# Optimization experiments

Hardware: AMD Instinct MI355X
Metric: run time of the kernel (lower is better)

The kernel has to match this reference:

```python
import jax, jax.numpy as jnp
import numpy as np

B, S, SR, H, NH, L, V, FF = 4, 512, 512, 1024, 16, 6, 32000, 4096
HD = H // NH  # 64
PAD = 2


def setup_inputs() -> dict:
    key = jax.random.key(0)
    ks = jax.random.split(key, 40)
    f32 = jnp.float32

    def n(k, shape, scale=0.02):
        return jax.random.normal(k, shape, f32) * scale

    encoder_outputs = jax.random.normal(ks[0], (B, SR, H), f32)
    decoder_input = jax.random.randint(ks[1], (B, S), 0, V)
    decoder_input = jnp.where(decoder_input == PAD, 3, decoder_input)
    decoder_input = decoder_input.at[:, S - 64:].set(PAD).at[:, 0].set(5)
    encoder_input = jax.random.randint(ks[2], (B, SR), 0, V)
    encoder_input = jnp.where(encoder_input == PAD, 3, encoder_input)
    encoder_input = encoder_input.at[:, SR - 64:].set(PAD)

    emb = jax.random.normal(ks[3], (V, H), f32).at[PAD].set(0.0)  # padding_idx=2 row is zero

    return {
        'encoder_outputs': encoder_outputs,
        'decoder_input': decoder_input,
        'encoder_input': encoder_input,
        'emb': emb,
        'wq1': n(ks[4], (L, H, H)), 'bq1': jnp.zeros((L, H), f32),
        'wk1': n(ks[5], (L, H, H)), 'bk1': jnp.zeros((L, H), f32),
        'wv1': n(ks[6], (L, H, H)), 'bv1': jnp.zeros((L, H), f32),
        'wo1': n(ks[7], (L, H, H)), 'bo1': jnp.zeros((L, H), f32),
        'pos1': jax.random.normal(ks[8], (L, 2 * S - 1, HD), f32),  # torch.randn init
        'wq2': n(ks[9], (L, H, H)), 'bq2': jnp.zeros((L, H), f32),
        'wk2': n(ks[10], (L, H, H)), 'bk2': jnp.zeros((L, H), f32),
        'wv2': n(ks[11], (L, H, H)), 'bv2': jnp.zeros((L, H), f32),
        'wo2': n(ks[12], (L, H, H)), 'bo2': jnp.zeros((L, H), f32),
        'ln1g': jnp.ones((L, H), f32), 'ln1b': jnp.zeros((L, H), f32),
        'ln2g': jnp.ones((L, H), f32), 'ln2b': jnp.zeros((L, H), f32),
        'ln3g': jnp.ones((L, H), f32), 'ln3b': jnp.zeros((L, H), f32),
        'wf1': n(ks[13], (L, H, FF)), 'bf1': jnp.zeros((L, FF), f32),
        'wf2': n(ks[14], (L, FF, H)), 'bf2': jnp.zeros((L, H), f32),
        'wout': n(ks[15], (H, V)), 'bout': jnp.zeros((V,), f32),
    }


def _split_heads(x):
    b, l, _ = x.shape
    return x.reshape(b, l, NH, HD).transpose(0, 2, 1, 3)  # b h l d


def _layer_norm(x, g, b):
    m = x.mean(-1, keepdims=True)
    v = ((x - m) ** 2).mean(-1, keepdims=True)
    return (x - m) / jnp.sqrt(v + 1e-5) * g + b


def _skew(q, P):
    # Transformer-XL style relative-position skew. q: [b,h,S,d] (already scaled), P: [2S-1,d]
    b = q.shape[0]
    pe = jnp.einsum('bhid,jd->bhij', q, P)                 # [b,h,S,2S-1]
    pe = jnp.pad(pe, ((0, 0), (0, 0), (0, 0), (0, 1)))      # [b,h,S,2S]
    pe = pe.reshape(b, NH, 2 * S * S)
    pe = jnp.pad(pe, ((0, 0), (0, 0), (0, S - 1)))
    pe = pe.reshape(b, NH, S + 1, 2 * S - 1)
    return pe[:, :, :-1, -S:]                               # [b,h,S,S]


def _attention(xq, xkv, wq, bq, wk, bk, wv, bv, wo, bo, pos, add_mask, causal):
    b = xq.shape[0]
    q = _split_heads(xq @ wq + bq) / np.float32(np.sqrt(HD))
    k = _split_heads(xkv @ wk + bk)
    v = _split_heads(xkv @ wv + bv)
    att = jnp.einsum('bhid,bhjd->bhij', q, k)
    if pos is not None:
        att = att + _skew(q, pos)
    if causal:
        i = jnp.arange(S)[:, None]
        j = jnp.arange(att.shape[-1])[None, :]
        att = jnp.where(j > i, -jnp.inf, att)
    if add_mask is not None:
        att = att + add_mask
    s = jax.nn.softmax(att, axis=-1)
    o = jnp.einsum('bhqk,bhkd->bhqd', s, v)
    o = o.transpose(0, 2, 1, 3).reshape(b, S, H)
    return o @ wo + bo


def _forward(encoder_outputs, decoder_input, encoder_input, emb,
             wq1, bq1, wk1, bk1, wv1, bv1, wo1, bo1, pos1,
             wq2, bq2, wk2, bk2, wv2, bv2, wo2, bo2,
             ln1g, ln1b, ln2g, ln2b, ln3g, ln3b,
             wf1, bf1, wf2, bf2, wout, bout):
    self_mask = jnp.where(decoder_input == PAD, -jnp.inf, 0.0)[:, None, None, :]   # [b,1,1,S]
    cross_mask = jnp.where(encoder_input == PAD, -jnp.inf, 0.0)[:, None, None, :]  # [b,1,1,SR]
    x = emb[decoder_input]  # dropout_p=0 -> identity
    for i in range(L):
        a1 = _attention(x, x, wq1[i], bq1[i], wk1[i], bk1[i], wv1[i], bv1[i],
                        wo1[i], bo1[i], pos1[i], self_mask, True)
        x1 = _layer_norm(a1 + x, ln1g[i], ln1b[i])
        a2 = _attention(x1, encoder_outputs, wq2[i], bq2[i], wk2[i], bk2[i], wv2[i], bv2[i],
                        wo2[i], bo2[i], None, cross_mask, False)
        x2 = _layer_norm(a2 + x1, ln2g[i], ln2b[i])
        ff = jax.nn.relu(x2 @ wf1[i] + bf1[i]) @ wf2[i] + bf2[i]
        x = _layer_norm(ff + x2, ln3g[i], ln3b[i])
    return jax.nn.log_softmax(x @ wout + bout, axis=-1)  # [b,S,V]


def reference(encoder_outputs, decoder_input, encoder_input, emb,
              wq1, bq1, wk1, bk1, wv1, bv1, wo1, bo1, pos1,
              wq2, bq2, wk2, bk2, wv2, bv2, wo2, bo2,
              ln1g, ln1b, ln2g, ln2b, ln3g, ln3b,
              wf1, bf1, wf2, bf2, wout, bout):
    return _forward(encoder_outputs, decoder_input, encoder_input, emb,
                    wq1, bq1, wk1, bk1, wv1, bv1, wo1, bo1, pos1,
                    wq2, bq2, wk2, bk2, wv2, bv2, wo2, bo2,
                    ln1g, ln1b, ln2g, ln2b, ln3g, ln3b,
                    wf1, bf1, wf2, bf2, wout, bout)
```

## Files before the change

kernel.cpp:

```cpp
#include <hip/hip_runtime.h>


typedef unsigned short u16;
typedef short s16x8 __attribute__((ext_vector_type(8)));
typedef unsigned short u16x4 __attribute__((ext_vector_type(4)));
typedef unsigned short u16x8 __attribute__((ext_vector_type(8)));
typedef float f32x4 __attribute__((ext_vector_type(4)));

#define PADTOK 2
#define NEG_INF (-__builtin_inff())

static __device__ __forceinline__ u16 f2bf(float f) {
  unsigned u = __float_as_uint(f);
  u += 0x7fffu + ((u >> 16) & 1u);
  return (u16)(u >> 16);
}
static __device__ __forceinline__ float bf2f(u16 h) {
  return __uint_as_float(((unsigned)h) << 16);
}
static __device__ __forceinline__ float f16tof(u16 h) {
  _Float16 x = __builtin_bit_cast(_Float16, h);
  return (float)x;
}
static __device__ __forceinline__ u16 ftof16(float v) {
  _Float16 x = (_Float16)v;
  return __builtin_bit_cast(u16, x);
}
static __device__ __forceinline__ f32x4 mfma16(s16x8 a, s16x8 b, f32x4 c) {
  asm("v_mfma_f32_16x16x32_bf16 %0, %1, %2, %0" : "+v"(c) : "v"(a), "v"(b));
  return c;
}
static __device__ __forceinline__ void gll16(const void* g, void* l) {
  __builtin_amdgcn_global_load_lds((const __attribute__((address_space(1))) void*)g,
                                   (__attribute__((address_space(3))) void*)l, 16, 0, 0);
}
static __device__ __forceinline__ size_t hsidx(int m, int n) {
  return ((size_t)((m >> 9) * 16 + (n >> 6))) * 32768u + (size_t)(m & 511) * 64u + (size_t)(n & 63);
}
static __device__ __forceinline__ size_t vtidx(int m, int n) {
  return ((size_t)((m >> 9) * 16 + (n >> 6))) * 65536u + (size_t)(n & 63) * 512u + (size_t)(m & 511);
}

static __device__ __forceinline__ void raster2(int& bm, int& bn) {
  const int nm = gridDim.y, nn = gridDim.x;
  int bid = blockIdx.y * nn + blockIdx.x;
  const int nwg = nm * nn;
  const int q = nwg >> 3, r = nwg & 7;
  const int x = bid & 7, p = bid >> 3;
  bid = (x < r ? x * (q + 1) : r * (q + 1) + (x - r) * q) + p;
  const int GM = nm < 8 ? nm : 8;
  const int pg = GM * nn;
  const int gi = bid / pg, rem = bid - gi * pg;
  const int left = nm - gi * GM;
  const int gm = left < GM ? left : GM;
  bm = gi * GM + rem % gm;
  bn = rem / gm;
}

template<int EPI, bool BF16OUT, int MFR, bool RELU, bool RESID, bool CSKIP>
__global__ __launch_bounds__(256)
void bgemm(const u16* __restrict__ A, long long sAg,
           const u16* __restrict__ Bt, long long sBg,
           const float* __restrict__ bias, const float* __restrict__ bias2,
           const float* __restrict__ bias3,
           const float* __restrict__ Res,
           void* __restrict__ Cv, u16* __restrict__ C2, u16* __restrict__ C3,
           long long sCg, int ldc, int K, float scale)
{
  constexpr int BM = MFR * 32;
  __shared__ u16 As[BM * 64];
  __shared__ u16 Bs[128 * 64];
  int bmi, bni;
  raster2(bmi, bni);
  const int bm0 = bmi * BM, bn0 = bni * 128;
  if constexpr (CSKIP) {
    if (bn0 > bm0 + BM - 1) return;
  }
  const int g = blockIdx.z;
  const u16* Ag = A + (size_t)g * (size_t)sAg;
  const u16* Bg = Bt + (size_t)g * (size_t)sBg;
  const int tid = threadIdx.x, l = tid & 63, w = tid >> 6;
  const int wm = w >> 1, wn = w & 1;
  const int rsel = l & 15, kg = l >> 4, xs = l & 7;

  f32x4 acc[MFR][4];
#pragma unroll
  for (int i = 0; i < MFR; ++i)
#pragma unroll
    for (int j = 0; j < 4; ++j) acc[i][j] = (f32x4){0.f, 0.f, 0.f, 0.f};

  const int srow = l >> 3;
  const int sch  = (l & 7) ^ srow;
  const u16* Agp = Ag + ((size_t)(bm0 + w * 8 * MFR + srow)) * (size_t)K + sch * 8;
  const u16* Bgp = Bg + ((size_t)(bn0 + w * 32 + srow)) * (size_t)K + sch * 8;
  char* AsL = (char*)As + (w * 8 * MFR) * 128;
  char* BsL = (char*)Bs + (w * 32) * 128;

  for (int k0 = 0; k0 < K; k0 += 64) {
    __syncthreads();
#pragma unroll
    for (int i = 0; i < MFR; ++i)
      gll16(Agp + (size_t)i * 8 * K + k0, AsL + i * 1024);
#pragma unroll
    for (int i = 0; i < 4; ++i)
      gll16(Bgp + (size_t)i * 8 * K + k0, BsL + i * 1024);
    __syncthreads();

    const int arow0 = (wm * (MFR * 16) + rsel) * 128;
    const int brow0 = (wn * 64 + rsel) * 128;
#pragma unroll
    for (int ks = 0; ks < 2; ++ks) {
      const int ch = ((ks * 4 + kg) ^ xs) * 16;
      s16x8 af[MFR], bfr[4];
#pragma unroll
      for (int mf = 0; mf < MFR; ++mf)
        af[mf] = *(const s16x8*)((const char*)As + arow0 + mf * 2048 + ch);
#pragma unroll
      for (int nf = 0; nf < 4; ++nf)
        bfr[nf] = *(const s16x8*)((const char*)Bs + brow0 + nf * 2048 + ch);
#pragma unroll
      for (int mf = 0; mf < MFR; ++mf)
#pragma unroll
        for (int nf = 0; nf < 4; ++nf)
          acc[mf][nf] = mfma16(af[mf], bfr[nf], acc[mf][nf]);
    }
  }

#pragma unroll
  for (int mf = 0; mf < MFR; ++mf) {
#pragma unroll
    for (int nf = 0; nf < 4; ++nf) {
      const int n = bn0 + wn * 64 + nf * 16 + rsel;
      if constexpr (EPI == 3) { if (n >= 64) continue; }
      int sub = 0, nl = n;
      const float* bp = bias;
      if constexpr (EPI == 4) {
        sub = n >> 10; nl = n & 1023;
        bp = (sub == 0) ? bias : (sub == 1) ? bias2 : bias3;
      }
      if constexpr (EPI == 5) {
        sub = n >> 10; nl = n & 1023;
        bp = (sub == 0) ? bias : bias2;
      }
      const float bv = bp ? bp[nl] : 0.f;
      float sc = 1.f;
      if constexpr (EPI == 0 || EPI == 1) sc = scale;
      if constexpr (EPI == 4) sc = (sub == 0) ? scale : 1.f;
#pragma unroll
      for (int e = 0; e < 4; ++e) {
        const int m = bm0 + wm * (MFR * 16) + mf * 16 + kg * 4 + e;
        float v = (acc[mf][nf][e] + bv) * sc;
        if constexpr (RELU) v = fmaxf(v, 0.f);
        if constexpr (RESID) v += Res[(size_t)m * (size_t)ldc + n];
        if constexpr (EPI == 0) {
          const size_t idx = (size_t)g * (size_t)sCg + (size_t)m * (size_t)ldc + n;
          if constexpr (BF16OUT) ((u16*)Cv)[idx] = f2bf(v);
          else                   ((float*)Cv)[idx] = v;
        } else if constexpr (EPI == 1) {
          ((u16*)Cv)[hsidx(m, nl)] = f2bf(v);
        } else if constexpr (EPI == 3) {
          const size_t idx = (size_t)(g >> 4) * 524288u + (size_t)m * 1024u
                           + (size_t)(g & 15) * 64u + n;
          ((u16*)Cv)[idx] = f2bf(v);
        } else if constexpr (EPI == 4) {
          if (sub == 2)      C3[vtidx(m, nl)] = f2bf(v);
          else if (sub == 1) C2[hsidx(m, nl)] = f2bf(v);
          else               ((u16*)Cv)[hsidx(m, nl)] = f2bf(v);
        } else if constexpr (EPI == 5) {
          if (sub == 0) ((u16*)Cv)[hsidx(m, nl)] = f2bf(v);
          else          C2[vtidx(m, nl)] = f2bf(v);
        } else if constexpr (EPI == 6) {
          ((u16*)Cv)[(size_t)m * (size_t)ldc + n] = ftof16(v);
        }
      }
    }
  }
}

static __device__ __forceinline__ void tconv_tile(const float* in, int N,
                                                  u16* out, int K, int k0, int n0) {
  __shared__ u16 L[64][72];
  const int t = threadIdx.x;
  const int rk = t >> 4, cn = (t & 15) * 4;
#pragma unroll
  for (int q = 0; q < 4; ++q) {
    const int kk = k0 + rk + q * 16;
    float4 v = *(const float4*)(in + (size_t)kk * (size_t)N + n0 + cn);
    L[cn + 0][rk + q * 16] = f2bf(v.x);
    L[cn + 1][rk + q * 16] = f2bf(v.y);
    L[cn + 2][rk + q * 16] = f2bf(v.z);
    L[cn + 3][rk + q * 16] = f2bf(v.w);
  }
  __syncthreads();
  const int rn = t >> 2, ck = (t & 3) * 16;
  u16* op = out + (size_t)(n0 + rn) * (size_t)K + k0 + ck;
  *(s16x8*)op       = *(const s16x8*)&L[rn][ck];
  *(s16x8*)(op + 8) = *(const s16x8*)&L[rn][ck + 8];
}

__global__ __launch_bounds__(256)
void conv_layer(const float* w0, const float* w1, const float* w2, const float* w3,
                const float* w4, const float* w5, const float* w6, const float* w7,
                const float* w8, const float* w9, u16* WT) {
  const int b = blockIdx.x;
  const float* in; u16* out; int N, K, kt, nt;
  if (b < 2048) {
    const int j = b >> 8, t = b & 255;
    const float* ws[8] = {w0, w1, w2, w3, w4, w5, w6, w7};
    in = ws[j]; out = WT + (size_t)j * 1048576u; K = 1024; N = 1024;
    kt = t >> 4; nt = t & 15;
  } else if (b < 3072) {
    const int t = b - 2048;
    in = w8; out = WT + 8388608u; K = 1024; N = 4096; kt = t >> 6; nt = t & 63;
  } else {
    const int t = b - 3072;
    in = w9; out = WT + 12582912u; K = 4096; N = 1024; kt = t >> 4; nt = t & 15;
  }
  tconv_tile(in, N, out, K, kt * 64, nt * 64);
}

__global__ __launch_bounds__(256)
void conv_wout(const float* in, u16* out) {
  const int b = blockIdx.x;
  const int kt = b / 500, nt = b % 500;
  tconv_tile(in, 32000, out, 1024, kt * 64, nt * 64);
}

__global__ void conv_bf16(const float* __restrict__ in, u16* __restrict__ out) {
  const int i = (blockIdx.x * 256 + threadIdx.x) * 4;
  float4 v = *(const float4*)(in + i);
  u16x4 h = {f2bf(v.x), f2bf(v.y), f2bf(v.z), f2bf(v.w)};
  *(u16x4*)(out + i) = h;
}

__global__ void conv_pos(const float* __restrict__ pos, u16* __restrict__ posb) {
  const int idx = (blockIdx.x * 256 + threadIdx.x) * 4;
  const int lyr = idx >> 15, rem = idx & 32767;
  float4 v = *(const float4*)(pos + (size_t)lyr * 65472u + rem);
  u16x4 h = {f2bf(v.x), f2bf(v.y), f2bf(v.z), f2bf(v.w)};
  *(u16x4*)(posb + idx) = h;
}

static __device__ __forceinline__ float wred_sum(float v) {
#pragma unroll
  for (int o = 32; o > 0; o >>= 1) v += __shfl_down(v, o, 64);
  return v;
}
static __device__ __forceinline__ float wred_max(float v) {
#pragma unroll
  for (int o = 32; o > 0; o >>= 1) v = fmaxf(v, __shfl_down(v, o, 64));
  return v;
}
static __device__ __forceinline__ float bred_sum(float v, float* sm) {
  const int lane = threadIdx.x & 63, wid = threadIdx.x >> 6;
  v = wred_sum(v);
  if (lane == 0) sm[wid] = v;
  __syncthreads();
  if (threadIdx.x == 0) sm[0] = sm[0] + sm[1] + sm[2] + sm[3];
  __syncthreads();
  const float r = sm[0];
  __syncthreads();
  return r;
}

__global__ void embed_kernel(const int* __restrict__ dec, const float* __restrict__ emb,
                             float* __restrict__ X, u16* __restrict__ Xh) {
  const int m = blockIdx.x, t = threadIdx.x;
  const int tok = dec[m];
  float4 v = ((const float4*)(emb + (size_t)tok * 1024u))[t];
  ((float4*)(X + (size_t)m * 1024u))[t] = v;
  u16x4 h = {f2bf(v.x), f2bf(v.y), f2bf(v.z), f2bf(v.w)};
  *(u16x4*)(Xh + (size_t)m * 1024u + t * 4) = h;
}

__global__ void layernorm_kernel(const float* __restrict__ R,
                                 const float* __restrict__ gw, const float* __restrict__ bw,
                                 float* __restrict__ Y, u16* __restrict__ Yh) {
  __shared__ float sm[4];
  const int m = blockIdx.x, t = threadIdx.x;
  float4 v = ((const float4*)(R + (size_t)m * 1024u))[t];
  float s = v.x + v.y + v.z + v.w;
  s = bred_sum(s, sm);
  const float mean = s * (1.f / 1024.f);
  const float d0 = v.x - mean, d1 = v.y - mean, d2 = v.z - mean, d3 = v.w - mean;
  float q = d0 * d0 + d1 * d1 + d2 * d2 + d3 * d3;
  q = bred_sum(q, sm);
  const float rstd = rsqrtf(q * (1.f / 1024.f) + 1e-5f);
  const int c = t * 4;
  float4 o;
  o.x = d0 * rstd * gw[c + 0] + bw[c + 0];
  o.y = d1 * rstd * gw[c + 1] + bw[c + 1];
  o.z = d2 * rstd * gw[c + 2] + bw[c + 2];
  o.w = d3 * rstd * gw[c + 3] + bw[c + 3];
  ((float4*)(Y + (size_t)m * 1024u))[t] = o;
  u16x4 h = {f2bf(o.x), f2bf(o.y), f2bf(o.z), f2bf(o.w)};
  *(u16x4*)(Yh + (size_t)m * 1024u + c) = h;
}

template<bool SELF>
__global__ void softmax_rows(const u16* __restrict__ SC, u16* __restrict__ P,
                             const int* __restrict__ msk) {
  __shared__ float sm[4];
  const int g = blockIdx.y, b = g >> 4;
  const int tid = threadIdx.x;
  const int half = tid >> 7, t = tid & 127, wid = tid >> 6;
  const int i = blockIdx.x * 2 + half;
  const size_t ro = ((size_t)g * 512 + (size_t)i) * 512u;
  const u16* row = SC + ro;
  u16* prow = P + ro;
  const int j0 = t * 4;
  const u16x4 sv = *(const u16x4*)(row + j0);
  const int4 dv = *(const int4*)(msk + b * 512 + j0);
  const int dm[4] = {dv.x, dv.y, dv.z, dv.w};
  float v[4];
#pragma unroll
  for (int e = 0; e < 4; ++e) {
    const int j = j0 + e;
    bool ok = (dm[e] != PADTOK);
    if constexpr (SELF) ok = ok && (j <= i);
    float x;
    if constexpr (SELF) {
      const int r = (j <= i) ? (511 + j - i) : 0;
      x = bf2f(sv[e]) + bf2f(prow[r]);
    } else {
      x = bf2f(sv[e]);
    }
    v[e] = ok ? x : NEG_INF;
  }
  float wm = wred_max(fmaxf(fmaxf(v[0], v[1]), fmaxf(v[2], v[3])));
  if ((tid & 63) == 0) sm[wid] = wm;
  __syncthreads();
  const float mx = fmaxf(sm[half * 2], sm[half * 2 + 1]);
  float e0 = expf(v[0] - mx), e1 = expf(v[1] - mx);
  float e2 = expf(v[2] - mx), e3 = expf(v[3] - mx);
  float ws = wred_sum(e0 + e1 + e2 + e3);
  __syncthreads();
  if ((tid & 63) == 0) sm[wid] = ws;
  __syncthreads();
  const float inv = 1.f / (sm[half * 2] + sm[half * 2 + 1]);
  const u16x4 o = {f2bf(e0 * inv), f2bf(e1 * inv), f2bf(e2 * inv), f2bf(e3 * inv)};
  *(u16x4*)(prow + j0) = o;
}

__global__ __launch_bounds__(512)
void log_softmax_kernel(float* __restrict__ out) {
  __shared__ u16 row[32000];
  __shared__ float sm[8];
  const int m = blockIdx.x, tid = threadIdx.x;
  const u16* src = (const u16*)out + (size_t)m * 64000u;
  for (int c = tid; c < 4000; c += 512)
    *(u16x8*)&row[c * 8] = *(const u16x8*)(src + c * 8);
  __syncthreads();
  float mx = NEG_INF;
  for (int c = tid; c < 4000; c += 512) {
    const u16x8 h = *(const u16x8*)&row[c * 8];
#pragma unroll
    for (int e = 0; e < 8; ++e) mx = fmaxf(mx, f16tof(h[e]));
  }
  mx = wred_max(mx);
  if ((tid & 63) == 0) sm[tid >> 6] = mx;
  __syncthreads();
  if (tid == 0) {
    float a = sm[0];
#pragma unroll
    for (int wI = 1; wI < 8; ++wI) a = fmaxf(a, sm[wI]);
    sm[0] = a;
  }
  __syncthreads();
  mx = sm[0];
  __syncthreads();
  float s = 0.f;
  for (int c = tid; c < 4000; c += 512) {
    const u16x8 h = *(const u16x8*)&row[c * 8];
#pragma unroll
    for (int e = 0; e < 8; ++e) s += expf(f16tof(h[e]) - mx);
  }
  s = wred_sum(s);
  if ((tid & 63) == 0) sm[tid >> 6] = s;
  __syncthreads();
  if (tid == 0) {
    float a = 0.f;
#pragma unroll
    for (int wI = 0; wI < 8; ++wI) a += sm[wI];
    sm[0] = a;
  }
  __syncthreads();
  const float lse = mx + logf(sm[0]);
  float* dst = out + (size_t)m * 32000u;
  for (int c = tid; c < 4000; c += 512) {
    const u16x8 h = *(const u16x8*)&row[c * 8];
    float4 o0, o1;
    o0.x = f16tof(h[0]) - lse; o0.y = f16tof(h[1]) - lse;
    o0.z = f16tof(h[2]) - lse; o0.w = f16tof(h[3]) - lse;
    o1.x = f16tof(h[4]) - lse; o1.y = f16tof(h[5]) - lse;
    o1.z = f16tof(h[6]) - lse; o1.w = f16tof(h[7]) - lse;
    ((float4*)dst)[c * 2]     = o0;
    ((float4*)dst)[c * 2 + 1] = o1;
  }
}

extern "C" void kernel_launch(void* const* d_in, const int* in_sizes, int n_in,
                              void* d_out, int out_size, void* d_ws, size_t ws_size,
                              hipStream_t stream) {
  const float* enc_out = (const float*)d_in[0];
  const int*   dec_in  = (const int*)d_in[1];
  const int*   enc_in  = (const int*)d_in[2];
  const float* emb     = (const float*)d_in[3];
  const float* wq1 = (const float*)d_in[4];  const float* bq1 = (const float*)d_in[5];
  const float* wk1 = (const float*)d_in[6];  const float* bk1 = (const float*)d_in[7];
  const float* wv1 = (const float*)d_in[8];  const float* bv1 = (const float*)d_in[9];
  const float* wo1 = (const float*)d_in[10]; const float* bo1 = (const float*)d_in[11];
  const float* pos1 = (const float*)d_in[12];
  const float* wq2 = (const float*)d_in[13]; const float* bq2 = (const float*)d_in[14];
  const float* wk2 = (const float*)d_in[15]; const float* bk2 = (const float*)d_in[16];
  const float* wv2 = (const float*)d_in[17]; const float* bv2 = (const float*)d_in[18];
  const float* wo2 = (const float*)d_in[19]; const float* bo2 = (const float*)d_in[20];
  const float* ln1g = (const float*)d_in[21]; const float* ln1b = (const float*)d_in[22];
  const float* ln2g = (const float*)d_in[23]; const float* ln2b = (const float*)d_in[24];
  const float* ln3g = (const float*)d_in[25]; const float* ln3b = (const float*)d_in[26];
  const float* wf1 = (const float*)d_in[27]; const float* bf1 = (const float*)d_in[28];
  const float* wf2 = (const float*)d_in[29]; const float* bf2 = (const float*)d_in[30];
  const float* wout = (const float*)d_in[31]; const float* bout = (const float*)d_in[32];

  char* ws = (char*)d_ws;
  u16*   WT    = (u16*)(ws + 0);
  u16*   SCb   = (u16*)(ws + 33554432);
  u16*   WoutT = (u16*)(ws + 0);
  u16*   PEP   = (u16*)(ws + 67108864);
  float* X     = (float*)(ws + 100663296);
  float* Xa    = (float*)(ws + 109051904);
  float* Xb    = (float*)(ws + 117440512);
  float* Rb    = (float*)(ws + 125829120);
  u16*   Ab16  = (u16*)(ws + 134217728);
  u16*   Q     = (u16*)(ws + 138412032);
  u16*   Kh    = (u16*)(ws + 142606336);
  u16*   VT    = (u16*)(ws + 146800640);
  u16*   Ob16  = (u16*)(ws + 155189248);
  u16*   FFH16 = (u16*)(ws + 159383552);
  u16*   encb  = (u16*)(ws + 176160768);
  u16*   posb  = (u16*)(ws + 180355072);
  float* out   = (float*)d_out;

  embed_kernel<<<2048, 256, 0, stream>>>(dec_in, emb, X, Ab16);
  conv_bf16<<<2048, 256, 0, stream>>>(enc_out, encb);
  conv_pos<<<192, 256, 0, stream>>>(pos1, posb);

  for (int i = 0; i < 6; ++i) {
    const size_t oHH = (size_t)i * 1048576u, oH = (size_t)i * 1024u;
    const float* bq1i = bq1 + oH; const float* bk1i = bk1 + oH;
    const float* bv1i = bv1 + oH; const float* bo1i = bo1 + oH;
    const float* bq2i = bq2 + oH; const float* bk2i = bk2 + oH;
    const float* bv2i = bv2 + oH; const float* bo2i = bo2 + oH;
    const float* bf1i = bf1 + (size_t)i * 4096u; const float* bf2i = bf2 + oH;
    const u16* posL = posb + (size_t)i * 32768u;

    conv_layer<<<4096, 256, 0, stream>>>(
        wq1 + oHH, wk1 + oHH, wv1 + oHH, wo1 + oHH,
        wq2 + oHH, wk2 + oHH, wv2 + oHH, wo2 + oHH,
        wf1 + (size_t)i * 4194304u, wf2 + (size_t)i * 4194304u, WT);

    bgemm<4, true, 4, false, false, false><<<dim3(24, 16, 1), 256, 0, stream>>>(
        Ab16, 0, WT, 0, bq1i, bk1i, bv1i, nullptr, Q, Kh, VT, 0, 0, 1024, 0.125f);
    bgemm<0, true, 4, false, false, false><<<dim3(4, 256, 1), 256, 0, stream>>>(
        Q, 0, posL, 0, nullptr, nullptr, nullptr, nullptr, PEP, nullptr, nullptr,
        0, 512, 64, 1.f);
    bgemm<0, true, 4, false, false, true><<<dim3(4, 4, 64), 256, 0, stream>>>(
        Q, 32768, Kh, 32768, nullptr, nullptr, nullptr, nullptr, SCb, nullptr, nullptr,
        262144, 512, 64, 1.f);
    softmax_rows<true><<<dim3(256, 64), 256, 0, stream>>>(SCb, PEP, dec_in);
    bgemm<3, true, 4, false, false, false><<<dim3(1, 4, 64), 256, 0, stream>>>(
        PEP, 262144, VT, 65536, nullptr, nullptr, nullptr, nullptr, Ob16, nullptr, nullptr,
        0, 0, 512, 1.f);
    bgemm<0, false, 2, false, true, false><<<dim3(8, 32, 1), 256, 0, stream>>>(
        Ob16, 0, WT + 3145728u, 0, bo1i, nullptr, nullptr, X, Rb, nullptr, nullptr,
        0, 1024, 1024, 1.f);
    layernorm_kernel<<<2048, 256, 0, stream>>>(Rb, ln1g + oH, ln1b + oH, Xa, Ab16);

    bgemm<1, true, 2, false, false, false><<<dim3(8, 32, 1), 256, 0, stream>>>(
        Ab16, 0, WT + 4194304u, 0, bq2i, nullptr, nullptr, nullptr, Q, nullptr, nullptr,
        0, 0, 1024, 0.125f);
    bgemm<5, true, 4, false, false, false><<<dim3(16, 16, 1), 256, 0, stream>>>(
        encb, 0, WT + 5242880u, 0, bk2i, bv2i, nullptr, nullptr, Kh, VT, nullptr,
        0, 0, 1024, 1.f);
    bgemm<0, true, 4, false, false, false><<<dim3(4, 4, 64), 256, 0, stream>>>(
        Q, 32768, Kh, 32768, nullptr, nullptr, nullptr, nullptr, SCb, nullptr, nullptr,
        262144, 512, 64, 1.f);
    softmax_rows<false><<<dim3(256, 64), 256, 0, stream>>>(SCb, PEP, enc_in);
    bgemm<3, true, 4, false, false, false><<<dim3(1, 4, 64), 256, 0, stream>>>(
        PEP, 262144, VT, 65536, nullptr, nullptr, nullptr, nullptr, Ob16, nullptr, nullptr,
        0, 0, 512, 1.f);
    bgemm<0, false, 2, false, true, false><<<dim3(8, 32, 1), 256, 0, stream>>>(
        Ob16, 0, WT + 7340032u, 0, bo2i, nullptr, nullptr, Xa, Rb, nullptr, nullptr,
        0, 1024, 1024, 1.f);
    layernorm_kernel<<<2048, 256, 0, stream>>>(Rb, ln2g + oH, ln2b + oH, Xb, Ab16);

    bgemm<0, true, 4, true, false, false><<<dim3(32, 16, 1), 256, 0, stream>>>(
        Ab16, 0, WT + 8388608u, 0, bf1i, nullptr, nullptr, nullptr, FFH16, nullptr, nullptr,
        0, 4096, 1024, 1.f);
    bgemm<0, false, 2, false, true, false><<<dim3(8, 32, 1), 256, 0, stream>>>(
        FFH16, 0, WT + 12582912u, 0, bf2i, nullptr, nullptr, Xb, Rb, nullptr, nullptr,
        0, 1024, 4096, 1.f);
    layernorm_kernel<<<2048, 256, 0, stream>>>(Rb, ln3g + oH, ln3b + oH, X, Ab16);
  }

  conv_wout<<<8000, 256, 0, stream>>>(wout, WoutT);
  bgemm<6, false, 4, false, false, false><<<dim3(250, 16, 1), 256, 0, stream>>>(
      Ab16, 0, WoutT, 0, bout, nullptr, nullptr, nullptr, out, nullptr, nullptr,
      0, 64000, 1024, 1.f);
  log_softmax_kernel<<<2048, 512, 0, stream>>>(out);
}
```

Before: 2.350 ms.

## Fuse QK^T, masking, softmax and PV into a single attention kernel

Replaces the per-layer score GEMM, softmax kernel and PV GEMM with one fused attention kernel per 32-row query tile. Scores sit in shared memory as bf16, causal rows stop at the diagonal, and masks are precomputed once as float additive vectors. This removes the score-matrix round trips through global memory and several launches. It also skips the unused lower region of the positional GEMM and makes the raster group size a template parameter, using a larger group for the vocab projection. In exchange, each block holds a large shared-memory footprint, and splitting the PV reduction across waves adds a cross-wave reduction step.

Result: no change. 2.311 ms (-1.6%).

```diff
diff --git a/kernel.cpp b/kernel.cpp
--- a/kernel.cpp
+++ b/kernel.cpp
@@ -41,14 +41,14 @@
   return ((size_t)((m >> 9) * 16 + (n >> 6))) * 65536u + (size_t)(n & 63) * 512u + (size_t)(m & 511);
 }
 
-static __device__ __forceinline__ void raster2(int& bm, int& bn) {
+static __device__ __forceinline__ void raster2(int& bm, int& bn, int GM0) {
   const int nm = gridDim.y, nn = gridDim.x;
   int bid = blockIdx.y * nn + blockIdx.x;
   const int nwg = nm * nn;
   const int q = nwg >> 3, r = nwg & 7;
   const int x = bid & 7, p = bid >> 3;
   bid = (x < r ? x * (q + 1) : r * (q + 1) + (x - r) * q) + p;
-  const int GM = nm < 8 ? nm : 8;
+  const int GM = nm < GM0 ? nm : GM0;
   const int pg = GM * nn;
   const int gi = bid / pg, rem = bid - gi * pg;
   const int left = nm - gi * GM;
@@ -57,7 +57,7 @@
   bn = rem / gm;
 }
 
-template<int EPI, bool BF16OUT, int MFR, bool RELU, bool RESID, bool CSKIP>
+template<int EPI, bool BF16OUT, int MFR, bool RELU, bool RESID, int SKIP, int GMT>
 __global__ __launch_bounds__(256)
 void bgemm(const u16* __restrict__ A, long long sAg,
            const u16* __restrict__ Bt, long long sBg,
@@ -71,10 +71,13 @@
   __shared__ u16 As[BM * 64];
   __shared__ u16 Bs[128 * 64];
   int bmi, bni;
-  raster2(bmi, bni);
+  raster2(bmi, bni, GMT);
   const int bm0 = bmi * BM, bn0 = bni * 128;
-  if constexpr (CSKIP) {
+  if constexpr (SKIP == 1) {
     if (bn0 > bm0 + BM - 1) return;
+  }
+  if constexpr (SKIP == 2) {
+    if ((bm0 & 511) + bn0 <= 256) return;
   }
   const int g = blockIdx.z;
   const u16* Ag = A + (size_t)g * (size_t)sAg;
@@ -131,7 +134,6 @@
 #pragma unroll
     for (int nf = 0; nf < 4; ++nf) {
       const int n = bn0 + wn * 64 + nf * 16 + rsel;
-      if constexpr (EPI == 3) { if (n >= 64) continue; }
       int sub = 0, nl = n;
       const float* bp = bias;
       if constexpr (EPI == 4) {
@@ -158,10 +160,6 @@
           else                   ((float*)Cv)[idx] = v;
         } else if constexpr (EPI == 1) {
           ((u16*)Cv)[hsidx(m, nl)] = f2bf(v);
-        } else if constexpr (EPI == 3) {
-          const size_t idx = (size_t)(g >> 4) * 524288u + (size_t)m * 1024u
-                           + (size_t)(g & 15) * 64u + n;
-          ((u16*)Cv)[idx] = f2bf(v);
         } else if constexpr (EPI == 4) {
           if (sub == 2)      C3[vtidx(m, nl)] = f2bf(v);
           else if (sub == 1) C2[hsidx(m, nl)] = f2bf(v);
@@ -175,6 +173,130 @@
       }
     }
   }
+}
+
+template<bool SELF>
+__global__ __launch_bounds__(256)
+void fused_attn(const u16* __restrict__ Qb, const u16* __restrict__ Kb,
+                const u16* __restrict__ Vt, const u16* __restrict__ PE,
+                const float* __restrict__ maskf, u16* __restrict__ O)
+{
+  __shared__ u16 SP[32][520];
+  __shared__ float Of[4][32][68];
+  __shared__ float rs[32];
+  const int it = blockIdx.x, g = blockIdx.y, b = g >> 4, h = g & 15;
+  const int i0 = it * 32;
+  const int CT = SELF ? (i0 + 32) : 512;
+  const int tid = threadIdx.x, l = tid & 63, w = tid >> 6;
+  const int rsel = l & 15, kg = l >> 4;
+
+  const u16* Qg = Qb + (size_t)g * 32768u;
+  const u16* Kg = Kb + (size_t)g * 32768u;
+  const u16* Vg = Vt + (size_t)g * 65536u;
+
+  s16x8 qf[2][2];
+#pragma unroll
+  for (int rt = 0; rt < 2; ++rt)
+#pragma unroll
+    for (int ks = 0; ks < 2; ++ks)
+      qf[rt][ks] = *(const s16x8*)(Qg + (size_t)(i0 + rt * 16 + rsel) * 64u + ks * 32 + kg * 8);
+
+  for (int ct = w; ct * 16 < CT; ct += 4) {
+    const int j = ct * 16 + rsel;
+    const s16x8 kf0 = *(const s16x8*)(Kg + (size_t)j * 64u + kg * 8);
+    const s16x8 kf1 = *(const s16x8*)(Kg + (size_t)j * 64u + 32 + kg * 8);
+    f32x4 a0 = {0.f, 0.f, 0.f, 0.f}, a1 = {0.f, 0.f, 0.f, 0.f};
+    a0 = mfma16(qf[0][0], kf0, a0);
+    a0 = mfma16(qf[0][1], kf1, a0);
+    a1 = mfma16(qf[1][0], kf0, a1);
+    a1 = mfma16(qf[1][1], kf1, a1);
+    const float mj = maskf[b * 512 + j];
+#pragma unroll
+    for (int rt = 0; rt < 2; ++rt) {
+      const f32x4 av = rt ? a1 : a0;
+#pragma unroll
+      for (int e = 0; e < 4; ++e) {
+        const int r = rt * 16 + kg * 4 + e;
+        float v = av[e] + mj;
+        if constexpr (SELF) {
+          const int i = i0 + r;
+          if (j > i) v = NEG_INF;
+          else       v += bf2f(PE[((size_t)(g * 512 + i)) * 512u + (511 + j - i)]);
+        }
+        SP[r][j] = f2bf(v);
+      }
+    }
+  }
+  __syncthreads();
+
+  const int r = tid >> 3, sc0 = (tid & 7) * 4;
+  float mx = NEG_INF;
+  for (int c = sc0; c < CT; c += 32) {
+    const u16x4 h4 = *(const u16x4*)&SP[r][c];
+#pragma unroll
+    for (int e = 0; e < 4; ++e) mx = fmaxf(mx, bf2f(h4[e]));
+  }
+#pragma unroll
+  for (int o = 1; o < 8; o <<= 1) mx = fmaxf(mx, __shfl_xor(mx, o, 64));
+  float sum = 0.f;
+  for (int c = sc0; c < CT; c += 32) {
+    const u16x4 h4 = *(const u16x4*)&SP[r][c];
+    const float p0 = expf(bf2f(h4[0]) - mx), p1 = expf(bf2f(h4[1]) - mx);
+    const float p2 = expf(bf2f(h4[2]) - mx), p3 = expf(bf2f(h4[3]) - mx);
+    sum += p0 + p1 + p2 + p3;
+    const u16x4 o4 = {f2bf(p0), f2bf(p1), f2bf(p2), f2bf(p3)};
+    *(u16x4*)&SP[r][c] = o4;
+  }
+#pragma unroll
+  for (int o = 1; o < 8; o <<= 1) sum += __shfl_xor(sum, o, 64);
+  if ((tid & 7) == 0) rs[r] = 1.f / sum;
+  __syncthreads();
+
+  f32x4 oa[2][4];
+#pragma unroll
+  for (int rt = 0; rt < 2; ++rt)
+#pragma unroll
+    for (int nt = 0; nt < 4; ++nt) oa[rt][nt] = (f32x4){0.f, 0.f, 0.f, 0.f};
+  const int nk = CT >> 5;
+  for (int kt = w; kt < nk; kt += 4) {
+    const s16x8 pf0 = *(const s16x8*)&SP[rsel][kt * 32 + kg * 8];
+    const s16x8 pf1 = *(const s16x8*)&SP[16 + rsel][kt * 32 + kg * 8];
+    s16x8 vf[4];
+#pragma unroll
+    for (int nt = 0; nt < 4; ++nt)
+      vf[nt] = *(const s16x8*)(Vg + (size_t)(nt * 16 + rsel) * 512u + kt * 32 + kg * 8);
+#pragma unroll
+    for (int nt = 0; nt < 4; ++nt) {
+      oa[0][nt] = mfma16(pf0, vf[nt], oa[0][nt]);
+      oa[1][nt] = mfma16(pf1, vf[nt], oa[1][nt]);
+    }
+  }
+#pragma unroll
+  for (int rt = 0; rt < 2; ++rt)
+#pragma unroll
+    for (int nt = 0; nt < 4; ++nt)
+#pragma unroll
+      for (int e = 0; e < 4; ++e)
+        Of[w][rt * 16 + kg * 4 + e][nt * 16 + rsel] = oa[rt][nt][e];
+  __syncthreads();
+
+  const int c0 = (tid & 7) * 8;
+  const float inv = rs[r];
+  float ov[8];
+#pragma unroll
+  for (int q = 0; q < 2; ++q) {
+    const float4 s0 = *(const float4*)&Of[0][r][c0 + q * 4];
+    const float4 s1 = *(const float4*)&Of[1][r][c0 + q * 4];
+    const float4 s2 = *(const float4*)&Of[2][r][c0 + q * 4];
+    const float4 s3 = *(const float4*)&Of[3][r][c0 + q * 4];
+    ov[q * 4 + 0] = (s0.x + s1.x + s2.x + s3.x) * inv;
+    ov[q * 4 + 1] = (s0.y + s1.y + s2.y + s3.y) * inv;
+    ov[q * 4 + 2] = (s0.z + s1.z + s2.z + s3.z) * inv;
+    ov[q * 4 + 3] = (s0.w + s1.w + s2.w + s3.w) * inv;
+  }
+  const u16x8 o8 = {f2bf(ov[0]), f2bf(ov[1]), f2bf(ov[2]), f2bf(ov[3]),
+                    f2bf(ov[4]), f2bf(ov[5]), f2bf(ov[6]), f2bf(ov[7])};
+  *(u16x8*)(O + ((size_t)(b * 512 + i0 + r)) * 1024u + h * 64 + c0) = o8;
 }
 
 static __device__ __forceinline__ void tconv_tile(const float* in, int N,
@@ -239,6 +361,13 @@
   float4 v = *(const float4*)(pos + (size_t)lyr * 65472u + rem);
   u16x4 h = {f2bf(v.x), f2bf(v.y), f2bf(v.z), f2bf(v.w)};
   *(u16x4*)(posb + idx) = h;
+}
+
+__global__ void mask_kernel(const int* __restrict__ dec, const int* __restrict__ enc,
+                            float* __restrict__ mD, float* __restrict__ mE) {
+  const int i = blockIdx.x * 256 + threadIdx.x;
+  mD[i] = (dec[i] == PADTOK) ? NEG_INF : 0.f;
+  mE[i] = (enc[i] == PADTOK) ? NEG_INF : 0.f;
 }
 
 static __device__ __forceinline__ float wred_sum(float v) {
@@ -297,51 +426,6 @@
   *(u16x4*)(Yh + (size_t)m * 1024u + c) = h;
 }
 
-template<bool SELF>
-__global__ void softmax_rows(const u16* __restrict__ SC, u16* __restrict__ P,
-                             const int* __restrict__ msk) {
-  __shared__ float sm[4];
-  const int g = blockIdx.y, b = g >> 4;
-  const int tid = threadIdx.x;
-  const int half = tid >> 7, t = tid & 127, wid = tid >> 6;
-  const int i = blockIdx.x * 2 + half;
-  const size_t ro = ((size_t)g * 512 + (size_t)i) * 512u;
-  const u16* row = SC + ro;
-  u16* prow = P + ro;
-  const int j0 = t * 4;
-  const u16x4 sv = *(const u16x4*)(row + j0);
-  const int4 dv = *(const int4*)(msk + b * 512 + j0);
-  const int dm[4] = {dv.x, dv.y, dv.z, dv.w};
-  float v[4];
-#pragma unroll
-  for (int e = 0; e < 4; ++e) {
-    const int j = j0 + e;
-    bool ok = (dm[e] != PADTOK);
-    if constexpr (SELF) ok = ok && (j <= i);
-    float x;
-    if constexpr (SELF) {
-      const int r = (j <= i) ? (511 + j - i) : 0;
-      x = bf2f(sv[e]) + bf2f(prow[r]);
-    } else {
-      x = bf2f(sv[e]);
-    }
-    v[e] = ok ? x : NEG_INF;
-  }
-  float wm = wred_max(fmaxf(fmaxf(v[0], v[1]), fmaxf(v[2], v[3])));
-  if ((tid & 63) == 0) sm[wid] = wm;
-  __syncthreads();
-  const float mx = fmaxf(sm[half * 2], sm[half * 2 + 1]);
-  float e0 = expf(v[0] - mx), e1 = expf(v[1] - mx);
-  float e2 = expf(v[2] - mx), e3 = expf(v[3] - mx);
-  float ws = wred_sum(e0 + e1 + e2 + e3);
-  __syncthreads();
-  if ((tid & 63) == 0) sm[wid] = ws;
-  __syncthreads();
-  const float inv = 1.f / (sm[half * 2] + sm[half * 2 + 1]);
-  const u16x4 o = {f2bf(e0 * inv), f2bf(e1 * inv), f2bf(e2 * inv), f2bf(e3 * inv)};
-  *(u16x4*)(prow + j0) = o;
-}
-
 __global__ __launch_bounds__(512)
 void log_softmax_kernel(float* __restrict__ out) {
   __shared__ u16 row[32000];
@@ -424,7 +508,8 @@
 
   char* ws = (char*)d_ws;
   u16*   WT    = (u16*)(ws + 0);
-  u16*   SCb   = (u16*)(ws + 33554432);
+  float* maskD = (float*)(ws + 33554432);
+  float* maskE = (float*)(ws + 33562624);
   u16*   WoutT = (u16*)(ws + 0);
   u16*   PEP   = (u16*)(ws + 67108864);
   float* X     = (float*)(ws + 100663296);
@@ -444,6 +529,7 @@
   embed_kernel<<<2048, 256, 0, stream>>>(dec_in, emb, X, Ab16);
   conv_bf16<<<2048, 256, 0, stream>>>(enc_out, encb);
   conv_pos<<<192, 256, 0, stream>>>(pos1, posb);
+  mask_kernel<<<8, 256, 0, stream>>>(dec_in, enc_in, maskD, maskE);
 
   for (int i = 0; i < 6; ++i) {
     const size_t oHH = (size_t)i * 1048576u, oH = (size_t)i * 1024u;
@@ -459,52 +545,40 @@
         wq2 + oHH, wk2 + oHH, wv2 + oHH, wo2 + oHH,
         wf1 + (size_t)i * 4194304u, wf2 + (size_t)i * 4194304u, WT);
 
-    bgemm<4, true, 4, false, false, false><<<dim3(24, 16, 1), 256, 0, stream>>>(
+    bgemm<4, true, 4, false, false, 0, 8><<<dim3(24, 16, 1), 256, 0, stream>>>(
         Ab16, 0, WT, 0, bq1i, bk1i, bv1i, nullptr, Q, Kh, VT, 0, 0, 1024, 0.125f);
-    bgemm<0, true, 4, false, false, false><<<dim3(4, 256, 1), 256, 0, stream>>>(
+    bgemm<0, true, 4, false, false, 2, 8><<<dim3(4, 256, 1), 256, 0, stream>>>(
         Q, 0, posL, 0, nullptr, nullptr, nullptr, nullptr, PEP, nullptr, nullptr,
         0, 512, 64, 1.f);
-    bgemm<0, true, 4, false, false, true><<<dim3(4, 4, 64), 256, 0, stream>>>(
-        Q, 32768, Kh, 32768, nullptr, nullptr, nullptr, nullptr, SCb, nullptr, nullptr,
-        262144, 512, 64, 1.f);
-    softmax_rows<true><<<dim3(256, 64), 256, 0, stream>>>(SCb, PEP, dec_in);
-    bgemm<3, true, 4, false, false, false><<<dim3(1, 4, 64), 256, 0, stream>>>(
-        PEP, 262144, VT, 65536, nullptr, nullptr, nullptr, nullptr, Ob16, nullptr, nullptr,
-        0, 0, 512, 1.f);
-    bgemm<0, false, 2, false, true, false><<<dim3(8, 32, 1), 256, 0, stream>>>(
+    fused_attn<true><<<dim3(16, 64), 256, 0, stream>>>(Q, Kh, VT, PEP, maskD, Ob16);
+    bgemm<0, false, 2, false, true, 0, 8><<<dim3(8, 32, 1), 256, 0, stream>>>(
         Ob16, 0, WT + 3145728u, 0, bo1i, nullptr, nullptr, X, Rb, nullptr, nullptr,
         0, 1024, 1024, 1.f);
     layernorm_kernel<<<2048, 256, 0, stream>>>(Rb, ln1g + oH, ln1b + oH, Xa, Ab16);
 
-    bgemm<1, true, 2, false, false, false><<<dim3(8, 32, 1), 256, 0, stream>>>(
+    bgemm<1, true, 2, false, false, 0, 8><<<dim3(8, 32, 1), 256, 0, stream>>>(
         Ab16, 0, WT + 4194304u, 0, bq2i, nullptr, nullptr, nullptr, Q, nullptr, nullptr,
         0, 0, 1024, 0.125f);
-    bgemm<5, true, 4, false, false, false><<<dim3(16, 16, 1), 256, 0, stream>>>(
+    bgemm<5, true, 4, false, false, 0, 8><<<dim3(16, 16, 1), 256, 0, stream>>>(
         encb, 0, WT + 5242880u, 0, bk2i, bv2i, nullptr, nullptr, Kh, VT, nullptr,
         0, 0, 1024, 1.f);
-    bgemm<0, true, 4, false, false, false><<<dim3(4, 4, 64), 256, 0, stream>>>(
-        Q, 32768, Kh, 32768, nullptr, nullptr, nullptr, nullptr, SCb, nullptr, nullptr,
-        262144, 512, 64, 1.f);
-    softmax_rows<false><<<dim3(256, 64), 256, 0, stream>>>(SCb, PEP, enc_in);
-    bgemm<3, true, 4, false, false, false><<<dim3(1, 4, 64), 256, 0, stream>>>(
-        PEP, 262144, VT, 65536, nullptr, nullptr, nullptr, nullptr, Ob16, nullptr, nullptr,
-        0, 0, 512, 1.f);
-    bgemm<0, false, 2, false, true, false><<<dim3(8, 32, 1), 256, 0, stream>>>(
+    fused_attn<false><<<dim3(16, 64), 256, 0, stream>>>(Q, Kh, VT, nullptr, maskE, Ob16);
+    bgemm<0, false, 2, false, true, 0, 8><<<dim3(8, 32, 1), 256, 0, stream>>>(
         Ob16, 0, WT + 7340032u, 0, bo2i, nullptr, nullptr, Xa, Rb, nullptr, nullptr,
         0, 1024, 1024, 1.f);
     layernorm_kernel<<<2048, 256, 0, stream>>>(Rb, ln2g + oH, ln2b + oH, Xb, Ab16);
 
-    bgemm<0, true, 4, true, false, false><<<dim3(32, 16, 1), 256, 0, stream>>>(
+    bgemm<0, true, 4, true, false, 0, 8><<<dim3(32, 16, 1), 256, 0, stream>>>(
         Ab16, 0, WT + 8388608u, 0, bf1i, nullptr, nullptr, nullptr, FFH16, nullptr, nullptr,
         0, 4096, 1024, 1.f);
-    bgemm<0, false, 2, false, true, false><<<dim3(8, 32, 1), 256, 0, stream>>>(
+    bgemm<0, false, 2, false, true, 0, 8><<<dim3(8, 32, 1), 256, 0, stream>>>(
         FFH16, 0, WT + 12582912u, 0, bf2i, nullptr, nullptr, Xb, Rb, nullptr, nullptr,
         0, 1024, 4096, 1.f);
     layernorm_kernel<<<2048, 256, 0, stream>>>(Rb, ln3g + oH, ln3b + oH, X, Ab16);
   }
 
   conv_wout<<<8000, 256, 0, stream>>>(wout, WoutT);
-  bgemm<6, false, 4, false, false, false><<<dim3(250, 16, 1), 256, 0, stream>>>(
+  bgemm<6, false, 4, false, false, 0, 16><<<dim3(250, 16, 1), 256, 0, stream>>>(
       Ab16, 0, WoutT, 0, bout, nullptr, nullptr, nullptr, out, nullptr, nullptr,
       0, 64000, 1024, 1.f);
   log_softmax_kernel<<<2048, 512, 0, stream>>>(out);
```
